# Kernel tuning notes

Measured on AMD Instinct MI355X. Metric: run time of the kernel, lower is better.

The kernel has to match this reference:

```python
import jax, jax.numpy as jnp
import numpy as np

B, S, D, H = 4, 2048, 1024, 16
DEPTH = D // H


def setup_inputs() -> dict:
    key = jax.random.key(0)
    ks = jax.random.split(key, 12)
    q = jax.random.normal(ks[0], (B, S, D), dtype=jnp.float32)
    k = jax.random.normal(ks[1], (B, S, D), dtype=jnp.float32)
    v = jax.random.normal(ks[2], (B, S, D), dtype=jnp.float32)
    # causal mask: 1.0 where attention is disallowed (upper triangle), per `mask * -1e9`
    mask = 1.0 - jnp.tril(jnp.ones((S, S), dtype=jnp.float32))
    mask = mask[None, None, :, :]  # [1,1,S,S] broadcastable over batch/heads
    scale = 1.0 / np.sqrt(D)
    Wq = jax.random.normal(ks[3], (D, D), dtype=jnp.float32) * scale
    Wk = jax.random.normal(ks[4], (D, D), dtype=jnp.float32) * scale
    Wv = jax.random.normal(ks[5], (D, D), dtype=jnp.float32) * scale
    Wo = jax.random.normal(ks[6], (D, D), dtype=jnp.float32) * scale
    bq = jnp.zeros((D,), jnp.float32)
    bk = jnp.zeros((D,), jnp.float32)
    bv = jnp.zeros((D,), jnp.float32)
    bo = jnp.zeros((D,), jnp.float32)
    return {"query": q, "key": k, "value": v, "mask": mask,
            "Wq": Wq, "bq": bq, "Wk": Wk, "bk": bk,
            "Wv": Wv, "bv": bv, "Wo": Wo, "bo": bo}


def _split_heads(x):
    # [B, S, D] -> [B, H, S, depth]
    b, s, _ = x.shape
    return x.reshape(b, s, H, DEPTH).transpose(0, 2, 1, 3)


def reference(query, key, value, mask, Wq, bq, Wk, bk, Wv, bv, Wo, bo):
    q = _split_heads(query @ Wq + bq)   # [B,H,S,depth]
    k = _split_heads(key @ Wk + bk)
    v = _split_heads(value @ Wv + bv)
    scores = jnp.einsum('bhqd,bhkd->bhqk', q, k) / jnp.sqrt(
        jnp.asarray(DEPTH, q.dtype))
    scores = scores + mask * (-1e9)
    attn = jax.nn.softmax(scores, axis=-1)
    out = jnp.einsum('bhqk,bhkd->bhqd', attn, v)   # [B,H,S,depth]
    out = out.transpose(0, 2, 1, 3).reshape(query.shape[0], -1, H * DEPTH)
    return out @ Wo + bo
```

## Files before the change

### kernel.cpp

```cpp
#include <hip/hip_runtime.h>

#define Bsz 4
#define SEQ 2048
#define DIM 1024
#define NH 16
#define HD 64

typedef float  f32x4  __attribute__((ext_vector_type(4)));
typedef __bf16 bf16x8 __attribute__((ext_vector_type(8)));
typedef __bf16 bf16x4 __attribute__((ext_vector_type(4)));
typedef short  s16x4  __attribute__((ext_vector_type(4)));

__device__ __forceinline__ f32x4 mfma16(bf16x8 a, bf16x8 b, f32x4 c) {
    return __builtin_amdgcn_mfma_f32_16x16x32_bf16(a, b, c, 0, 0, 0);
}
__device__ __forceinline__ f32x4 mfma16k16(bf16x4 a, bf16x4 b, f32x4 c) {
#if defined(__has_builtin) && __has_builtin(__builtin_amdgcn_mfma_f32_16x16x16bf16_1k)
    return __builtin_amdgcn_mfma_f32_16x16x16bf16_1k(
        __builtin_bit_cast(s16x4, a), __builtin_bit_cast(s16x4, b), c, 0, 0, 0);
#else
    asm volatile("s_nop 2\n\tv_mfma_f32_16x16x16_bf16 %0, %1, %2, %0\n\ts_nop 7\n\ts_nop 7"
                 : "+v"(c) : "v"(a), "v"(b));
    return c;
#endif
}

#define GLD_LDS16(gsrc, ldst)                                                        \
    __builtin_amdgcn_global_load_lds(                                                \
        (const __attribute__((address_space(1))) void*)(gsrc),                       \
        (__attribute__((address_space(3))) void*)(ldst), 16, 0, 0)

__global__ __launch_bounds__(256) void wt_kernel(
    const float* __restrict__ Wq, const float* __restrict__ Wk,
    const float* __restrict__ Wv, const float* __restrict__ Wo,
    __bf16* __restrict__ wt)
{
    __shared__ float tile[64][65];
    int z = blockIdx.z;
    const float* W = (z == 0) ? Wq : (z == 1) ? Wk : (z == 2) ? Wv : Wo;
    __bf16* out = wt + (size_t)z * DIM * DIM;
    int kb = blockIdx.x * 64, nb = blockIdx.y * 64;
    int t = threadIdx.x;
    int cidx = t & 63, ridx = t >> 6;
#pragma unroll
    for (int i = 0; i < 16; i++) {
        int r = ridx + i * 4;
        tile[r][cidx] = W[(size_t)(kb + r) * DIM + nb + cidx];
    }
    __syncthreads();
#pragma unroll
    for (int i = 0; i < 16; i++) {
        int r = ridx + i * 4;
        out[(size_t)(nb + r) * DIM + kb + cidx] = (__bf16)tile[cidx][r];
    }
}

__global__ __launch_bounds__(256, 2) void gemm_proj(
    const float* __restrict__ Xq, const float* __restrict__ Xk,
    const float* __restrict__ Xv, const __bf16* __restrict__ wt,
    const float* __restrict__ bq, const float* __restrict__ bk,
    const float* __restrict__ bv,
    __bf16* __restrict__ oq, __bf16* __restrict__ ok, __bf16* __restrict__ ovT)
{
    int z = blockIdx.z;
    const float*  X    = (z == 0) ? Xq : (z == 1) ? Xk : Xv;
    const float*  bias = (z == 0) ? bq : (z == 1) ? bk : bv;
    const __bf16* Bt   = wt + (size_t)z * DIM * DIM;

    __shared__ __align__(16) char smem[36864];
    __bf16* const Ab = (__bf16*)smem;
    __bf16* const Bb = (__bf16*)(smem + 16384);

    int m0 = blockIdx.x * 128, n0 = blockIdx.y * 128;
    int tid = threadIdx.x, lane = tid & 63, w = tid >> 6;
    int c = lane & 15, g = lane >> 4;
    int wm = (w >> 1) * 64, wn = (w & 1) * 64;

    f32x4 acc[4][4] = {};

    int ar = tid >> 1, ah = tid & 1;
    const float* aptr = X + (size_t)(m0 + ar) * DIM + ah * 16;
    int awo = ar * 32 + ah * 16;

    int brow0 = (w * 2) * 16 + (lane >> 2);
    int bcol  = (lane & 3) * 8;
    const __bf16* bptr0 = Bt + (size_t)(n0 + brow0) * DIM + bcol;
    const __bf16* bptr1 = bptr0 + (size_t)16 * DIM;
    int bwo0 = (w * 2) * 512;
    int bwo1 = (w * 2 + 1) * 512;

    {
        f32x4 f0 = *(const f32x4*)(aptr);
        f32x4 f1 = *(const f32x4*)(aptr + 4);
        f32x4 f2 = *(const f32x4*)(aptr + 8);
        f32x4 f3 = *(const f32x4*)(aptr + 12);
        GLD_LDS16(bptr0, Bb + bwo0);
        GLD_LDS16(bptr1, Bb + bwo1);
        bf16x8 b0, b1;
#pragma unroll
        for (int j = 0; j < 4; j++) {
            b0[j]     = (__bf16)f0[j];
            b0[4 + j] = (__bf16)f1[j];
            b1[j]     = (__bf16)f2[j];
            b1[4 + j] = (__bf16)f3[j];
        }
        *(bf16x8*)(Ab + awo)     = b0;
        *(bf16x8*)(Ab + awo + 8) = b1;
    }
    __syncthreads();

    int cur = 0;
    for (int kt = 0; kt < 32; ++kt) {
        int nxt = kt + 1;
        int nb = cur ^ 1;
        f32x4 f0, f1, f2, f3;
        if (nxt < 32) {
            const float* ap = aptr + nxt * 32;
            f0 = *(const f32x4*)(ap);
            f1 = *(const f32x4*)(ap + 4);
            f2 = *(const f32x4*)(ap + 8);
            f3 = *(const f32x4*)(ap + 12);
            GLD_LDS16(bptr0 + nxt * 32, Bb + nb * 4096 + bwo0);
            GLD_LDS16(bptr1 + nxt * 32, Bb + nb * 4096 + bwo1);
        }
        bf16x8 af[4], bf[4];
#pragma unroll
        for (int mf = 0; mf < 4; mf++)
            af[mf] = *(bf16x8*)&Ab[cur * 4096 + (wm + mf * 16 + c) * 32 + g * 8];
#pragma unroll
        for (int nf = 0; nf < 4; nf++)
            bf[nf] = *(bf16x8*)&Bb[cur * 4096 + (wn + nf * 16 + c) * 32 + g * 8];
#pragma unroll
        for (int mf = 0; mf < 4; mf++)
#pragma unroll
            for (int nf = 0; nf < 4; nf++)
                acc[mf][nf] = mfma16(af[mf], bf[nf], acc[mf][nf]);
        if (nxt < 32) {
            bf16x8 b0, b1;
#pragma unroll
            for (int j = 0; j < 4; j++) {
                b0[j]     = (__bf16)f0[j];
                b0[4 + j] = (__bf16)f1[j];
                b1[j]     = (__bf16)f2[j];
                b1[4 + j] = (__bf16)f3[j];
            }
            *(bf16x8*)(Ab + nb * 4096 + awo)     = b0;
            *(bf16x8*)(Ab + nb * 4096 + awo + 8) = b1;
        }
        __syncthreads();
        cur = nb;
    }

    if (z == 2) {
        __bf16* T = (__bf16*)smem + (size_t)w * 4608;
#pragma unroll
        for (int nf = 0; nf < 4; nf++) {
            int col = n0 + wn + nf * 16 + c;
            int d = nf * 16 + c;
            float bval = bias[col];
#pragma unroll
            for (int mf = 0; mf < 4; mf++) {
                int sl = mf * 16 + g * 4;
                bf16x4 pk;
#pragma unroll
                for (int r = 0; r < 4; r++) pk[r] = (__bf16)(acc[mf][nf][r] + bval);
                *(bf16x4*)&T[d * 72 + sl] = pk;
            }
        }
        int h = (n0 + wn) >> 6;
        int bb = m0 >> 11;
        int s_base = (m0 & (SEQ - 1)) + wm;
        int dd = lane >> 2;
        int ss = (lane & 3) * 8;
        size_t obase = ((size_t)(bb * NH + h) * HD) * SEQ;
#pragma unroll
        for (int dgrp = 0; dgrp < 4; dgrp++)
#pragma unroll
            for (int half = 0; half < 2; half++) {
                int d = dgrp * 16 + dd;
                int s = half * 32 + ss;
                bf16x8 vv = *(bf16x8*)&T[d * 72 + s];
                *(bf16x8*)&ovT[obase + (size_t)d * SEQ + s_base + s] = vv;
            }
    } else {
        __bf16* Out = (z == 0) ? oq : ok;
#pragma unroll
        for (int nf = 0; nf < 4; nf++) {
            int col = n0 + wn + nf * 16 + c;
            float bval = bias[col];
#pragma unroll
            for (int mf = 0; mf < 4; mf++) {
                int row = m0 + wm + mf * 16 + g * 4;
#pragma unroll
                for (int r = 0; r < 4; r++)
                    Out[(size_t)(row + r) * DIM + col] = (__bf16)(acc[mf][nf][r] + bval);
            }
        }
    }
}

#define QSCALE 0.180336880f

__global__ __launch_bounds__(256, 2) void fa_kernel(
    const __bf16* __restrict__ qp, const __bf16* __restrict__ kp,
    const __bf16* __restrict__ vpT, __bf16* __restrict__ op)
{
    int bz = blockIdx.x;
    int bh = bz & 63;
    int b = bh >> 4, h = bh & 15;
    int qt = 15 - (bz >> 6);
    int q0 = qt * 128;

    int tid = threadIdx.x, lane = tid & 63, w = tid >> 6;
    int c = lane & 15, g = lane >> 4;

    __shared__ __bf16 Kbuf[64 * 64];
    __shared__ __bf16 Vbuf[64 * 64];

    const int qb[2] = {q0 + w * 16, q0 + 64 + w * 16};

    bf16x8 qf[2][2];
#pragma unroll
    for (int nq = 0; nq < 2; nq++) {
        const __bf16* qbase = qp + (size_t)(b * SEQ + qb[nq] + c) * DIM + h * HD;
#pragma unroll
        for (int kc = 0; kc < 2; kc++) {
            bf16x8 raw = *(const bf16x8*)(qbase + kc * 32 + g * 8);
            bf16x8 sc;
#pragma unroll
            for (int j = 0; j < 8; j++) sc[j] = (__bf16)((float)raw[j] * QSCALE);
            qf[nq][kc] = sc;
        }
    }

    f32x4 acc[4][2] = {};
    float m_run[2] = {-1e30f, -1e30f};
    float l_run[2] = {0.f, 0.f};

    int r8 = tid >> 3, c8 = tid & 7;
    int sch = c8 ^ (r8 & 7);
    const __bf16* kbase = kp  + (size_t)(b * SEQ + r8) * DIM + h * HD + sch * 8;
    const __bf16* vbase = vpT + ((size_t)(b * NH + h) * HD + r8) * SEQ + sch * 8;
    __bf16* kdst0 = Kbuf + w * 512;
    __bf16* kdst1 = Kbuf + 2048 + w * 512;
    __bf16* vdst0 = Vbuf + w * 512;
    __bf16* vdst1 = Vbuf + 2048 + w * 512;

    int vb4[4];
#pragma unroll
    for (int mkey = 0; mkey < 4; mkey++)
        vb4[mkey] = c * 64 + (((2 * mkey + (g >> 1)) ^ (c & 7)) * 8) + (g & 1) * 4;

    int ktmax = (q0 >> 6) + 2;
    for (int kt = 0; kt < ktmax; ++kt) {
        GLD_LDS16(kbase + (size_t)kt * 64 * DIM, kdst0);
        GLD_LDS16(kbase + (size_t)(kt * 64 + 32) * DIM, kdst1);
        GLD_LDS16(vbase + kt * 64, vdst0);
        GLD_LDS16(vbase + kt * 64 + (size_t)32 * SEQ, vdst1);
        __syncthreads();

        bool need0 = (kt * 64 <= qb[0] + 15);
        int kb0 = kt * 64;

        f32x4 s[4][2] = {};
#pragma unroll
        for (int kc = 0; kc < 2; kc++) {
            bf16x8 kf[4];
#pragma unroll
            for (int mkey = 0; mkey < 4; mkey++)
                kf[mkey] = *(bf16x8*)&Kbuf[(mkey * 16 + c) * 64 + (((kc * 4 + g) ^ (c & 7)) * 8)];
#pragma unroll
            for (int mkey = 0; mkey < 4; mkey++) {
                if (need0) s[mkey][0] = mfma16(kf[mkey], qf[0][kc], s[mkey][0]);
                s[mkey][1] = mfma16(kf[mkey], qf[1][kc], s[mkey][1]);
            }
        }

        bf16x4 pf[4][2];
#pragma unroll
        for (int nq = 0; nq < 2; nq++) {
            if (nq == 0 && !need0) continue;
            int qg = qb[nq] + c;
            if (kb0 + 63 > qg) {
#pragma unroll
                for (int mkey = 0; mkey < 4; mkey++)
#pragma unroll
                    for (int r2 = 0; r2 < 4; r2++)
                        if (kb0 + mkey * 16 + g * 4 + r2 > qg) s[mkey][nq][r2] = -1e30f;
            }
            float pm0 = fmaxf(fmaxf(s[0][nq][0], s[0][nq][1]), fmaxf(s[0][nq][2], s[0][nq][3]));
            float pm1 = fmaxf(fmaxf(s[1][nq][0], s[1][nq][1]), fmaxf(s[1][nq][2], s[1][nq][3]));
            float pm2 = fmaxf(fmaxf(s[2][nq][0], s[2][nq][1]), fmaxf(s[2][nq][2], s[2][nq][3]));
            float pm3 = fmaxf(fmaxf(s[3][nq][0], s[3][nq][1]), fmaxf(s[3][nq][2], s[3][nq][3]));
            float pm = fmaxf(fmaxf(pm0, pm1), fmaxf(pm2, pm3));
            pm = fmaxf(pm, __shfl_xor(pm, 16));
            pm = fmaxf(pm, __shfl_xor(pm, 32));
            float mo = m_run[nq];
            float mn = fmaxf(mo, pm);
            m_run[nq] = mn;
            float scl = exp2f(mo - mn);
            l_run[nq] *= scl;
#pragma unroll
            for (int nf = 0; nf < 4; nf++) acc[nf][nq] *= scl;
            float rs = 0.f;
#pragma unroll
            for (int mkey = 0; mkey < 4; mkey++) {
                bf16x4 pk;
#pragma unroll
                for (int r2 = 0; r2 < 4; r2++) {
                    float p = exp2f(s[mkey][nq][r2] - mn);
                    rs += p;
                    pk[r2] = (__bf16)p;
                }
                pf[mkey][nq] = pk;
            }
            rs += __shfl_xor(rs, 16);
            rs += __shfl_xor(rs, 32);
            l_run[nq] += rs;
        }

#pragma unroll
        for (int mkey = 0; mkey < 4; mkey++) {
#pragma unroll
            for (int nf = 0; nf < 4; nf++) {
                bf16x4 vf = *(bf16x4*)&Vbuf[vb4[mkey] + nf * 1024];
                if (need0) acc[nf][0] = mfma16k16(vf, pf[mkey][0], acc[nf][0]);
                acc[nf][1] = mfma16k16(vf, pf[mkey][1], acc[nf][1]);
            }
        }
        __syncthreads();
    }

#pragma unroll
    for (int nq = 0; nq < 2; nq++) {
        float inv = 1.f / l_run[nq];
        int row = qb[nq] + c;
        __bf16* obase = op + (size_t)(b * SEQ + row) * DIM + h * HD + g * 4;
#pragma unroll
        for (int nf = 0; nf < 4; nf++) {
            bf16x4 pk;
#pragma unroll
            for (int r2 = 0; r2 < 4; r2++) pk[r2] = (__bf16)(acc[nf][nq][r2] * inv);
            *(bf16x4*)(obase + nf * 16) = pk;
        }
    }
}

__global__ __launch_bounds__(256, 2) void gemm_out(
    const __bf16* __restrict__ Ain, const __bf16* __restrict__ wt,
    const float* __restrict__ bias, float* __restrict__ Out)
{
    const __bf16* Bt = wt + (size_t)3 * DIM * DIM;

    __shared__ __bf16 Ab[2][4096];
    __shared__ __bf16 Bb[2][4096];

    int m0 = blockIdx.x * 128, n0 = blockIdx.y * 128;
    int tid = threadIdx.x, lane = tid & 63, w = tid >> 6;
    int c = lane & 15, g = lane >> 4;
    int wm = (w >> 1) * 64, wn = (w & 1) * 64;

    f32x4 acc[4][4] = {};

    int srow = (w * 2) * 16 + (lane >> 2);
    int scol = (lane & 3) * 8;
    const __bf16* aptr0 = Ain + (size_t)(m0 + srow) * DIM + scol;
    const __bf16* aptr1 = aptr0 + (size_t)16 * DIM;
    const __bf16* bptr0 = Bt + (size_t)(n0 + srow) * DIM + scol;
    const __bf16* bptr1 = bptr0 + (size_t)16 * DIM;
    int so0 = (w * 2) * 512;
    int so1 = (w * 2 + 1) * 512;

    GLD_LDS16(aptr0, Ab[0] + so0);
    GLD_LDS16(aptr1, Ab[0] + so1);
    GLD_LDS16(bptr0, Bb[0] + so0);
    GLD_LDS16(bptr1, Bb[0] + so1);
    __syncthreads();

    int cur = 0;
    for (int kt = 0; kt < 32; ++kt) {
        int nxt = kt + 1;
        int nb = cur ^ 1;
        if (nxt < 32) {
            int k0 = nxt * 32;
            GLD_LDS16(aptr0 + k0, Ab[nb] + so0);
            GLD_LDS16(aptr1 + k0, Ab[nb] + so1);
            GLD_LDS16(bptr0 + k0, Bb[nb] + so0);
            GLD_LDS16(bptr1 + k0, Bb[nb] + so1);
        }
        bf16x8 af[4], bf[4];
#pragma unroll
        for (int mf = 0; mf < 4; mf++)
            af[mf] = *(bf16x8*)&Ab[cur][(wm + mf * 16 + c) * 32 + g * 8];
#pragma unroll
        for (int nf = 0; nf < 4; nf++)
            bf[nf] = *(bf16x8*)&Bb[cur][(wn + nf * 16 + c) * 32 + g * 8];
#pragma unroll
        for (int mf = 0; mf < 4; mf++)
#pragma unroll
            for (int nf = 0; nf < 4; nf++)
                acc[mf][nf] = mfma16(af[mf], bf[nf], acc[mf][nf]);
        __syncthreads();
        cur = nb;
    }

#pragma unroll
    for (int nf = 0; nf < 4; nf++) {
        int col = n0 + wn + nf * 16 + c;
        float bval = bias[col];
#pragma unroll
        for (int mf = 0; mf < 4; mf++) {
            int row = m0 + wm + mf * 16 + g * 4;
#pragma unroll
            for (int r = 0; r < 4; r++)
                Out[(size_t)(row + r) * DIM + col] = acc[mf][nf][r] + bval;
        }
    }
}

extern "C" void kernel_launch(void* const* d_in, const int* in_sizes, int n_in,
                              void* d_out, int out_size, void* d_ws, size_t ws_size,
                              hipStream_t stream)
{
    const float* q  = (const float*)d_in[0];
    const float* k  = (const float*)d_in[1];
    const float* v  = (const float*)d_in[2];
    const float* Wq = (const float*)d_in[4];
    const float* bq = (const float*)d_in[5];
    const float* Wk = (const float*)d_in[6];
    const float* bk = (const float*)d_in[7];
    const float* Wv = (const float*)d_in[8];
    const float* bv = (const float*)d_in[9];
    const float* Wo = (const float*)d_in[10];
    const float* bo = (const float*)d_in[11];

    char* ws = (char*)d_ws;
    __bf16* wt  = (__bf16*)ws;
    __bf16* qp  = (__bf16*)(ws + (size_t)(8u  << 20));
    __bf16* kp  = (__bf16*)(ws + (size_t)(24u << 20));
    __bf16* vpT = (__bf16*)(ws + (size_t)(40u << 20));
    __bf16* ao  = (__bf16*)(ws + (size_t)(56u << 20));

    wt_kernel<<<dim3(16, 16, 4), 256, 0, stream>>>(Wq, Wk, Wv, Wo, wt);
    gemm_proj<<<dim3(64, 8, 3), 256, 0, stream>>>(q, k, v, wt, bq, bk, bv, qp, kp, vpT);
    fa_kernel<<<dim3(1024), 256, 0, stream>>>(qp, kp, vpT, ao);
    gemm_out<<<dim3(64, 8), 256, 0, stream>>>(ao, wt, bo, (float*)d_out);

    (void)in_sizes; (void)n_in; (void)out_size; (void)ws_size;
}
```

Measured before the change: 201.1 us.

## Retile flash attention to 64-query/128-key blocks and stage fp32 A via LDS DMA

The projection GEMM now loads fp32 activations straight into swizzled LDS with global_load_lds and converts them to bf16 at fragment-read time, removing register staging and the conversion-store step. The V-transpose epilogue is split into halves so it needs less LDS. The attention kernel moves to 64-query blocks with 128-key tiles, doubling the grid and using one query fragment per wave. It also adds a lazy rescale of the softmax running max (skipped when the new max is within 8), a hardware exp2 intrinsic and s_setprio around the MFMA sections. The tradeoffs are larger LDS use, per-tile K/V reloads shared by fewer queries, and more conversion work in the GEMM inner loop.

Result: faster. 176.8 us (-12.0%).

```diff
diff --git a/kernel.cpp b/kernel.cpp
--- a/kernel.cpp
+++ b/kernel.cpp
@@ -22,6 +22,14 @@
     asm volatile("s_nop 2\n\tv_mfma_f32_16x16x16_bf16 %0, %1, %2, %0\n\ts_nop 7\n\ts_nop 7"
                  : "+v"(c) : "v"(a), "v"(b));
     return c;
+#endif
+}
+
+__device__ __forceinline__ float fast_exp2(float x) {
+#if defined(__has_builtin) && __has_builtin(__builtin_amdgcn_exp2f)
+    return __builtin_amdgcn_exp2f(x);
+#else
+    return exp2f(x);
 #endif
 }
 
@@ -67,9 +75,9 @@
     const float*  bias = (z == 0) ? bq : (z == 1) ? bk : bv;
     const __bf16* Bt   = wt + (size_t)z * DIM * DIM;
 
-    __shared__ __align__(16) char smem[36864];
-    __bf16* const Ab = (__bf16*)smem;
-    __bf16* const Bb = (__bf16*)(smem + 16384);
+    __shared__ __align__(16) char smem[49152];
+    float*  const Af = (float*)smem;
+    __bf16* const Bb = (__bf16*)(smem + 32768);
 
     int m0 = blockIdx.x * 128, n0 = blockIdx.y * 128;
     int tid = threadIdx.x, lane = tid & 63, w = tid >> 6;
@@ -78,55 +86,47 @@
 
     f32x4 acc[4][4] = {};
 
-    int ar = tid >> 1, ah = tid & 1;
-    const float* aptr = X + (size_t)(m0 + ar) * DIM + ah * 16;
-    int awo = ar * 32 + ah * 16;
-
-    int brow0 = (w * 2) * 16 + (lane >> 2);
-    int bcol  = (lane & 3) * 8;
-    const __bf16* bptr0 = Bt + (size_t)(n0 + brow0) * DIM + bcol;
+    int ar = tid >> 3, ach = tid & 7;
+    int asch = ach ^ (ar & 7);
+    const float* aptr = X + (size_t)(m0 + ar) * DIM + asch * 4;
+    int srow = (w * 2) * 16 + (lane >> 2);
+    int scol = (lane & 3) * 8;
+    const __bf16* bptr0 = Bt + (size_t)(n0 + srow) * DIM + scol;
     const __bf16* bptr1 = bptr0 + (size_t)16 * DIM;
-    int bwo0 = (w * 2) * 512;
-    int bwo1 = (w * 2 + 1) * 512;
-
-    {
-        f32x4 f0 = *(const f32x4*)(aptr);
-        f32x4 f1 = *(const f32x4*)(aptr + 4);
-        f32x4 f2 = *(const f32x4*)(aptr + 8);
-        f32x4 f3 = *(const f32x4*)(aptr + 12);
-        GLD_LDS16(bptr0, Bb + bwo0);
-        GLD_LDS16(bptr1, Bb + bwo1);
-        bf16x8 b0, b1;
-#pragma unroll
-        for (int j = 0; j < 4; j++) {
-            b0[j]     = (__bf16)f0[j];
-            b0[4 + j] = (__bf16)f1[j];
-            b1[j]     = (__bf16)f2[j];
-            b1[4 + j] = (__bf16)f3[j];
-        }
-        *(bf16x8*)(Ab + awo)     = b0;
-        *(bf16x8*)(Ab + awo + 8) = b1;
-    }
+    int so0 = (w * 2) * 512;
+    int so1 = (w * 2 + 1) * 512;
+
+#define STAGE_PROJ(buf, k0)                                                      \
+    do {                                                                         \
+        GLD_LDS16(aptr + (k0),                     Af + (buf) * 4096 + w * 256); \
+        GLD_LDS16(aptr + (k0) + (size_t)32 * DIM,  Af + (buf) * 4096 + 1024 + w * 256); \
+        GLD_LDS16(aptr + (k0) + (size_t)64 * DIM,  Af + (buf) * 4096 + 2048 + w * 256); \
+        GLD_LDS16(aptr + (k0) + (size_t)96 * DIM,  Af + (buf) * 4096 + 3072 + w * 256); \
+        GLD_LDS16(bptr0 + (k0),                    Bb + (buf) * 4096 + so0);     \
+        GLD_LDS16(bptr1 + (k0),                    Bb + (buf) * 4096 + so1);     \
+    } while (0)
+
+    STAGE_PROJ(0, 0);
     __syncthreads();
 
     int cur = 0;
     for (int kt = 0; kt < 32; ++kt) {
         int nxt = kt + 1;
         int nb = cur ^ 1;
-        f32x4 f0, f1, f2, f3;
-        if (nxt < 32) {
-            const float* ap = aptr + nxt * 32;
-            f0 = *(const f32x4*)(ap);
-            f1 = *(const f32x4*)(ap + 4);
-            f2 = *(const f32x4*)(ap + 8);
-            f3 = *(const f32x4*)(ap + 12);
-            GLD_LDS16(bptr0 + nxt * 32, Bb + nb * 4096 + bwo0);
-            GLD_LDS16(bptr1 + nxt * 32, Bb + nb * 4096 + bwo1);
-        }
+        if (nxt < 32) STAGE_PROJ(nb, nxt * 32);
+
         bf16x8 af[4], bf[4];
 #pragma unroll
-        for (int mf = 0; mf < 4; mf++)
-            af[mf] = *(bf16x8*)&Ab[cur * 4096 + (wm + mf * 16 + c) * 32 + g * 8];
+        for (int mf = 0; mf < 4; mf++) {
+            int arow = wm + mf * 16 + c;
+            const float* ap = &Af[cur * 4096 + arow * 32];
+            f32x4 a0 = *(const f32x4*)(ap + (((2 * g)     ^ (c & 7)) << 2));
+            f32x4 a1 = *(const f32x4*)(ap + (((2 * g + 1) ^ (c & 7)) << 2));
+            bf16x8 v;
+#pragma unroll
+            for (int j = 0; j < 4; j++) { v[j] = (__bf16)a0[j]; v[4 + j] = (__bf16)a1[j]; }
+            af[mf] = v;
+        }
 #pragma unroll
         for (int nf = 0; nf < 4; nf++)
             bf[nf] = *(bf16x8*)&Bb[cur * 4096 + (wn + nf * 16 + c) * 32 + g * 8];
@@ -135,38 +135,13 @@
 #pragma unroll
             for (int nf = 0; nf < 4; nf++)
                 acc[mf][nf] = mfma16(af[mf], bf[nf], acc[mf][nf]);
-        if (nxt < 32) {
-            bf16x8 b0, b1;
-#pragma unroll
-            for (int j = 0; j < 4; j++) {
-                b0[j]     = (__bf16)f0[j];
-                b0[4 + j] = (__bf16)f1[j];
-                b1[j]     = (__bf16)f2[j];
-                b1[4 + j] = (__bf16)f3[j];
-            }
-            *(bf16x8*)(Ab + nb * 4096 + awo)     = b0;
-            *(bf16x8*)(Ab + nb * 4096 + awo + 8) = b1;
-        }
         __syncthreads();
         cur = nb;
     }
+#undef STAGE_PROJ
 
     if (z == 2) {
-        __bf16* T = (__bf16*)smem + (size_t)w * 4608;
-#pragma unroll
-        for (int nf = 0; nf < 4; nf++) {
-            int col = n0 + wn + nf * 16 + c;
-            int d = nf * 16 + c;
-            float bval = bias[col];
-#pragma unroll
-            for (int mf = 0; mf < 4; mf++) {
-                int sl = mf * 16 + g * 4;
-                bf16x4 pk;
-#pragma unroll
-                for (int r = 0; r < 4; r++) pk[r] = (__bf16)(acc[mf][nf][r] + bval);
-                *(bf16x4*)&T[d * 72 + sl] = pk;
-            }
-        }
+        __bf16* T = (__bf16*)smem + (size_t)w * 2304;
         int h = (n0 + wn) >> 6;
         int bb = m0 >> 11;
         int s_base = (m0 & (SEQ - 1)) + wm;
@@ -174,14 +149,28 @@
         int ss = (lane & 3) * 8;
         size_t obase = ((size_t)(bb * NH + h) * HD) * SEQ;
 #pragma unroll
-        for (int dgrp = 0; dgrp < 4; dgrp++)
-#pragma unroll
-            for (int half = 0; half < 2; half++) {
+        for (int half = 0; half < 2; half++) {
+#pragma unroll
+            for (int mh = 0; mh < 2; mh++) {
+                int mf = half * 2 + mh;
+#pragma unroll
+                for (int nf = 0; nf < 4; nf++) {
+                    int col = n0 + wn + nf * 16 + c;
+                    int d = nf * 16 + c;
+                    float bval = bias[col];
+                    bf16x4 pk;
+#pragma unroll
+                    for (int r = 0; r < 4; r++) pk[r] = (__bf16)(acc[mf][nf][r] + bval);
+                    *(bf16x4*)&T[d * 36 + mh * 16 + g * 4] = pk;
+                }
+            }
+#pragma unroll
+            for (int dgrp = 0; dgrp < 4; dgrp++) {
                 int d = dgrp * 16 + dd;
-                int s = half * 32 + ss;
-                bf16x8 vv = *(bf16x8*)&T[d * 72 + s];
-                *(bf16x8*)&ovT[obase + (size_t)d * SEQ + s_base + s] = vv;
-            }
+                bf16x8 vv = *(bf16x8*)&T[d * 36 + ss];
+                *(bf16x8*)&ovT[obase + (size_t)d * SEQ + s_base + half * 32 + ss] = vv;
+            }
+        }
     } else {
         __bf16* Out = (z == 0) ? oq : ok;
 #pragma unroll
@@ -208,139 +197,146 @@
     int bz = blockIdx.x;
     int bh = bz & 63;
     int b = bh >> 4, h = bh & 15;
-    int qt = 15 - (bz >> 6);
-    int q0 = qt * 128;
+    int qt = 31 - (bz >> 6);
+    int q0 = qt * 64;
 
     int tid = threadIdx.x, lane = tid & 63, w = tid >> 6;
     int c = lane & 15, g = lane >> 4;
 
-    __shared__ __bf16 Kbuf[64 * 64];
-    __shared__ __bf16 Vbuf[64 * 64];
-
-    const int qb[2] = {q0 + w * 16, q0 + 64 + w * 16};
-
-    bf16x8 qf[2][2];
-#pragma unroll
-    for (int nq = 0; nq < 2; nq++) {
-        const __bf16* qbase = qp + (size_t)(b * SEQ + qb[nq] + c) * DIM + h * HD;
+    __shared__ __bf16 Kbuf[128 * 64];
+    __shared__ __bf16 Vbuf[64 * 128];
+
+    const int qg = q0 + w * 16 + c;
+
+    bf16x8 qf[2];
+    {
+        const __bf16* qbase = qp + (size_t)(b * SEQ + qg) * DIM + h * HD;
 #pragma unroll
         for (int kc = 0; kc < 2; kc++) {
             bf16x8 raw = *(const bf16x8*)(qbase + kc * 32 + g * 8);
             bf16x8 sc;
 #pragma unroll
             for (int j = 0; j < 8; j++) sc[j] = (__bf16)((float)raw[j] * QSCALE);
-            qf[nq][kc] = sc;
-        }
-    }
-
-    f32x4 acc[4][2] = {};
-    float m_run[2] = {-1e30f, -1e30f};
-    float l_run[2] = {0.f, 0.f};
-
-    int r8 = tid >> 3, c8 = tid & 7;
-    int sch = c8 ^ (r8 & 7);
-    const __bf16* kbase = kp  + (size_t)(b * SEQ + r8) * DIM + h * HD + sch * 8;
-    const __bf16* vbase = vpT + ((size_t)(b * NH + h) * HD + r8) * SEQ + sch * 8;
-    __bf16* kdst0 = Kbuf + w * 512;
-    __bf16* kdst1 = Kbuf + 2048 + w * 512;
-    __bf16* vdst0 = Vbuf + w * 512;
-    __bf16* vdst1 = Vbuf + 2048 + w * 512;
-
-    int vb4[4];
-#pragma unroll
-    for (int mkey = 0; mkey < 4; mkey++)
-        vb4[mkey] = c * 64 + (((2 * mkey + (g >> 1)) ^ (c & 7)) * 8) + (g & 1) * 4;
-
-    int ktmax = (q0 >> 6) + 2;
+            qf[kc] = sc;
+        }
+    }
+
+    f32x4 acc[4] = {};
+    float m_run = -1e30f;
+    float l_run = 0.f;
+
+    int kr = tid >> 3, kch = tid & 7;
+    int ksch = kch ^ (kr & 7);
+    const __bf16* kbase = kp + (size_t)(b * SEQ + kr) * DIM + h * HD + ksch * 8;
+    int vr = tid >> 4, vch = tid & 15;
+    int vsch = vch ^ (vr & 7);
+    const __bf16* vbase = vpT + ((size_t)(b * NH + h) * HD + vr) * SEQ + vsch * 8;
+
+    int vb4[8];
+#pragma unroll
+    for (int mkey = 0; mkey < 8; mkey++)
+        vb4[mkey] = c * 128 + (((2 * mkey + (g >> 1)) ^ (c & 7)) * 8) + (g & 1) * 4;
+
+    int ktmax = (qt >> 1) + 1;
     for (int kt = 0; kt < ktmax; ++kt) {
-        GLD_LDS16(kbase + (size_t)kt * 64 * DIM, kdst0);
-        GLD_LDS16(kbase + (size_t)(kt * 64 + 32) * DIM, kdst1);
-        GLD_LDS16(vbase + kt * 64, vdst0);
-        GLD_LDS16(vbase + kt * 64 + (size_t)32 * SEQ, vdst1);
+        const __bf16* kln = kbase + (size_t)kt * 128 * DIM;
+        const __bf16* vln = vbase + kt * 128;
+        GLD_LDS16(kln,                       Kbuf + w * 512);
+        GLD_LDS16(kln + (size_t)32 * DIM,    Kbuf + 2048 + w * 512);
+        GLD_LDS16(kln + (size_t)64 * DIM,    Kbuf + 4096 + w * 512);
+        GLD_LDS16(kln + (size_t)96 * DIM,    Kbuf + 6144 + w * 512);
+        GLD_LDS16(vln,                       Vbuf + w * 512);
+        GLD_LDS16(vln + (size_t)16 * SEQ,    Vbuf + 2048 + w * 512);
+        GLD_LDS16(vln + (size_t)32 * SEQ,    Vbuf + 4096 + w * 512);
+        GLD_LDS16(vln + (size_t)48 * SEQ,    Vbuf + 6144 + w * 512);
         __syncthreads();
 
-        bool need0 = (kt * 64 <= qb[0] + 15);
-        int kb0 = kt * 64;
-
-        f32x4 s[4][2] = {};
+        int kb0 = kt * 128;
+
+        f32x4 s[8] = {};
+        __builtin_amdgcn_s_setprio(1);
 #pragma unroll
         for (int kc = 0; kc < 2; kc++) {
-            bf16x8 kf[4];
-#pragma unroll
-            for (int mkey = 0; mkey < 4; mkey++)
-                kf[mkey] = *(bf16x8*)&Kbuf[(mkey * 16 + c) * 64 + (((kc * 4 + g) ^ (c & 7)) * 8)];
-#pragma unroll
-            for (int mkey = 0; mkey < 4; mkey++) {
-                if (need0) s[mkey][0] = mfma16(kf[mkey], qf[0][kc], s[mkey][0]);
-                s[mkey][1] = mfma16(kf[mkey], qf[1][kc], s[mkey][1]);
-            }
-        }
-
-        bf16x4 pf[4][2];
-#pragma unroll
-        for (int nq = 0; nq < 2; nq++) {
-            if (nq == 0 && !need0) continue;
-            int qg = qb[nq] + c;
-            if (kb0 + 63 > qg) {
-#pragma unroll
-                for (int mkey = 0; mkey < 4; mkey++)
-#pragma unroll
-                    for (int r2 = 0; r2 < 4; r2++)
-                        if (kb0 + mkey * 16 + g * 4 + r2 > qg) s[mkey][nq][r2] = -1e30f;
-            }
-            float pm0 = fmaxf(fmaxf(s[0][nq][0], s[0][nq][1]), fmaxf(s[0][nq][2], s[0][nq][3]));
-            float pm1 = fmaxf(fmaxf(s[1][nq][0], s[1][nq][1]), fmaxf(s[1][nq][2], s[1][nq][3]));
-            float pm2 = fmaxf(fmaxf(s[2][nq][0], s[2][nq][1]), fmaxf(s[2][nq][2], s[2][nq][3]));
-            float pm3 = fmaxf(fmaxf(s[3][nq][0], s[3][nq][1]), fmaxf(s[3][nq][2], s[3][nq][3]));
-            float pm = fmaxf(fmaxf(pm0, pm1), fmaxf(pm2, pm3));
-            pm = fmaxf(pm, __shfl_xor(pm, 16));
-            pm = fmaxf(pm, __shfl_xor(pm, 32));
-            float mo = m_run[nq];
-            float mn = fmaxf(mo, pm);
-            m_run[nq] = mn;
-            float scl = exp2f(mo - mn);
-            l_run[nq] *= scl;
-#pragma unroll
-            for (int nf = 0; nf < 4; nf++) acc[nf][nq] *= scl;
-            float rs = 0.f;
-#pragma unroll
-            for (int mkey = 0; mkey < 4; mkey++) {
-                bf16x4 pk;
-#pragma unroll
-                for (int r2 = 0; r2 < 4; r2++) {
-                    float p = exp2f(s[mkey][nq][r2] - mn);
-                    rs += p;
-                    pk[r2] = (__bf16)p;
-                }
-                pf[mkey][nq] = pk;
-            }
-            rs += __shfl_xor(rs, 16);
-            rs += __shfl_xor(rs, 32);
-            l_run[nq] += rs;
-        }
-
-#pragma unroll
-        for (int mkey = 0; mkey < 4; mkey++) {
+#pragma unroll
+            for (int mh = 0; mh < 2; mh++) {
+                bf16x8 kf[4];
+#pragma unroll
+                for (int mq = 0; mq < 4; mq++)
+                    kf[mq] = *(bf16x8*)&Kbuf[((mh * 4 + mq) * 16 + c) * 64 + (((kc * 4 + g) ^ (c & 7)) * 8)];
+#pragma unroll
+                for (int mq = 0; mq < 4; mq++)
+                    s[mh * 4 + mq] = mfma16(kf[mq], qf[kc], s[mh * 4 + mq]);
+            }
+        }
+        __builtin_amdgcn_s_setprio(0);
+
+        if (kb0 + 127 > qg) {
+#pragma unroll
+            for (int mkey = 0; mkey < 8; mkey++)
+#pragma unroll
+                for (int r2 = 0; r2 < 4; r2++)
+                    if (kb0 + mkey * 16 + g * 4 + r2 > qg) s[mkey][r2] = -1e30f;
+        }
+
+        float fm0 = fmaxf(fmaxf(s[0][0], s[0][1]), fmaxf(s[0][2], s[0][3]));
+        float fm1 = fmaxf(fmaxf(s[1][0], s[1][1]), fmaxf(s[1][2], s[1][3]));
+        float fm2 = fmaxf(fmaxf(s[2][0], s[2][1]), fmaxf(s[2][2], s[2][3]));
+        float fm3 = fmaxf(fmaxf(s[3][0], s[3][1]), fmaxf(s[3][2], s[3][3]));
+        float fm4 = fmaxf(fmaxf(s[4][0], s[4][1]), fmaxf(s[4][2], s[4][3]));
+        float fm5 = fmaxf(fmaxf(s[5][0], s[5][1]), fmaxf(s[5][2], s[5][3]));
+        float fm6 = fmaxf(fmaxf(s[6][0], s[6][1]), fmaxf(s[6][2], s[6][3]));
+        float fm7 = fmaxf(fmaxf(s[7][0], s[7][1]), fmaxf(s[7][2], s[7][3]));
+        float pm = fmaxf(fmaxf(fmaxf(fm0, fm1), fmaxf(fm2, fm3)),
+                         fmaxf(fmaxf(fm4, fm5), fmaxf(fm6, fm7)));
+        pm = fmaxf(pm, __shfl_xor(pm, 16));
+        pm = fmaxf(pm, __shfl_xor(pm, 32));
+        if (!__all(pm <= m_run + 8.f)) {
+            float mn = fmaxf(m_run, pm);
+            float scl = fast_exp2(m_run - mn);
+            l_run *= scl;
+#pragma unroll
+            for (int nf = 0; nf < 4; nf++) acc[nf] *= scl;
+            m_run = mn;
+        }
+        f32x4 rsv = {0.f, 0.f, 0.f, 0.f};
+        bf16x4 pf[8];
+#pragma unroll
+        for (int mkey = 0; mkey < 8; mkey++) {
+            bf16x4 pk;
+#pragma unroll
+            for (int r2 = 0; r2 < 4; r2++) {
+                float p = fast_exp2(s[mkey][r2] - m_run);
+                rsv[r2] += p;
+                pk[r2] = (__bf16)p;
+            }
+            pf[mkey] = pk;
+        }
+        float rs = (rsv[0] + rsv[1]) + (rsv[2] + rsv[3]);
+        rs += __shfl_xor(rs, 16);
+        rs += __shfl_xor(rs, 32);
+        l_run += rs;
+
+        __builtin_amdgcn_s_setprio(1);
+#pragma unroll
+        for (int mkey = 0; mkey < 8; mkey++) {
 #pragma unroll
             for (int nf = 0; nf < 4; nf++) {
-                bf16x4 vf = *(bf16x4*)&Vbuf[vb4[mkey] + nf * 1024];
-                if (need0) acc[nf][0] = mfma16k16(vf, pf[mkey][0], acc[nf][0]);
-                acc[nf][1] = mfma16k16(vf, pf[mkey][1], acc[nf][1]);
-            }
-        }
+                bf16x4 vf = *(bf16x4*)&Vbuf[vb4[mkey] + nf * 2048];
+                acc[nf] = mfma16k16(vf, pf[mkey], acc[nf]);
+            }
+        }
+        __builtin_amdgcn_s_setprio(0);
         __syncthreads();
     }
 
-#pragma unroll
-    for (int nq = 0; nq < 2; nq++) {
-        float inv = 1.f / l_run[nq];
-        int row = qb[nq] + c;
-        __bf16* obase = op + (size_t)(b * SEQ + row) * DIM + h * HD + g * 4;
+    {
+        float inv = 1.f / l_run;
+        __bf16* obase = op + (size_t)(b * SEQ + qg) * DIM + h * HD + g * 4;
 #pragma unroll
         for (int nf = 0; nf < 4; nf++) {
             bf16x4 pk;
 #pragma unroll
-            for (int r2 = 0; r2 < 4; r2++) pk[r2] = (__bf16)(acc[nf][nq][r2] * inv);
+            for (int r2 = 0; r2 < 4; r2++) pk[r2] = (__bf16)(acc[nf][r2] * inv);
             *(bf16x4*)(obase + nf * 16) = pk;
         }
     }
@@ -443,7 +439,7 @@
 
     wt_kernel<<<dim3(16, 16, 4), 256, 0, stream>>>(Wq, Wk, Wv, Wo, wt);
     gemm_proj<<<dim3(64, 8, 3), 256, 0, stream>>>(q, k, v, wt, bq, bk, bv, qp, kp, vpT);
-    fa_kernel<<<dim3(1024), 256, 0, stream>>>(qp, kp, vpT, ao);
+    fa_kernel<<<dim3(2048), 256, 0, stream>>>(qp, kp, vpT, ao);
     gemm_out<<<dim3(64, 8), 256, 0, stream>>>(ao, wt, bo, (float*)d_out);
 
     (void)in_sizes; (void)n_in; (void)out_size; (void)ws_size;
```
